# Kernel tuning notes

Measured on AMD Instinct MI355X. Metric: run time of the kernel, lower is better.

Reference implementation:

```python
import jax, jax.numpy as jnp
import numpy as np

EPS = 1e-6
N_HEADS = 16
D_HEAD = 64

def _rmsnorm(x, scale):
    rms = jnp.sqrt(jnp.mean(x * x, axis=-1, keepdims=True) + EPS)
    return x / rms * scale

def setup_inputs() -> dict:
    key = jax.random.key(0)
    ks = jax.random.split(key, 8)
    B, L, D = 512, 64, 1024
    return {
        "x": jax.random.normal(ks[0], (B, L, D), dtype=jnp.float32),
        "rel_indices": jax.random.randint(ks[1], (L, L), 0, 225, dtype=jnp.int64),
        "Wq": jax.random.normal(ks[2], (D, D), dtype=jnp.float32) * 0.02,
        "Wk": jax.random.normal(ks[3], (D, D), dtype=jnp.float32) * 0.02,
        "Wv": jax.random.normal(ks[4], (D, D), dtype=jnp.float32) * 0.02,
        "Wo": jax.random.normal(ks[5], (D, D), dtype=jnp.float32) * 0.02,
        "q_scale": jnp.ones((D_HEAD,), dtype=jnp.float32),
        "k_scale": jnp.ones((D_HEAD,), dtype=jnp.float32),
        "rel_k": jax.random.normal(ks[6], (225, D_HEAD), dtype=jnp.float32) * 0.02,
        "rel_v": jax.random.normal(ks[7], (225, D_HEAD), dtype=jnp.float32) * 0.02,
    }

def reference(x, rel_indices, Wq, Wk, Wv, Wo, q_scale, k_scale, rel_k, rel_v):
    B, L, D = x.shape
    H, dk = N_HEADS, D_HEAD
    scale = 1.0 / jnp.sqrt(jnp.float32(dk))
    # projections; Linear with weight W applied as x @ W (bias=False)
    q = (x @ Wq).reshape(B, L, H, dk)
    k = (x @ Wk).reshape(B, L, H, dk)
    v = (x @ Wv).reshape(B, L, H, dk).transpose(0, 2, 1, 3)  # bhld
    q = _rmsnorm(q, q_scale).transpose(0, 2, 1, 3)  # bhld
    k = _rmsnorm(k, k_scale).transpose(0, 2, 1, 3)  # bhld
    r_k = rel_k[rel_indices]  # [L, L, dk]
    r_v = rel_v[rel_indices]  # [L, L, dk]
    content = jnp.einsum('bhid,bhjd->bhij', q, k)
    rel = jnp.einsum('bhid,ijd->bhij', q, r_k)
    probs = jax.nn.softmax((content + rel) * scale, axis=-1)
    out = jnp.einsum('bhij,bhjd->bhid', probs, v) + jnp.einsum('bhij,ijd->bhid', probs, r_v)
    out = out.transpose(0, 2, 1, 3).reshape(B, L, D)
    return out @ Wo
```

## Files before the change

kernel.cpp:

```cpp
#include <hip/hip_runtime.h>
#include <stdint.h>

typedef unsigned short u16;
typedef __attribute__((ext_vector_type(8))) short s16x8;
typedef __attribute__((ext_vector_type(4))) float f32x4;

#define DEV static __device__ __forceinline__

#define MFMA16(a, b, c) __builtin_amdgcn_mfma_f32_16x16x32_bf16((a), (b), (c), 0, 0, 0)

DEV u16 f2b(float f) {
  unsigned u = __float_as_uint(f);
  unsigned r = (u + 0x7fffu + ((u >> 16) & 1u)) >> 16;
  return (u16)r;
}
DEV float b2f(u16 u) { return __uint_as_float(((unsigned)u) << 16); }

typedef const __attribute__((address_space(1))) unsigned int* as1p;
typedef __attribute__((address_space(3))) unsigned int* as3p;

DEV void gload16(const void* g, void* l) {
  __builtin_amdgcn_global_load_lds((as1p)(uintptr_t)g, (as3p)(unsigned)(uintptr_t)l, 16, 0, 0);
}

DEV void ldsPkAddBf16(void* ldsPtr, unsigned packed) {
  unsigned addr = (unsigned)(uintptr_t)ldsPtr;
  asm volatile("ds_pk_add_bf16 %0, %1" : : "v"(addr), "v"(packed) : "memory");
}

__global__ void conv_x_k(const float* __restrict__ x, u16* __restrict__ xb) {
  const int n8 = 32768 * 1024 / 8;
  int i = blockIdx.x * 256 + threadIdx.x;
  int stride = gridDim.x * 256;
  for (; i < n8; i += stride) {
    const float4* p = (const float4*)x + (size_t)i * 2;
    float4 a = p[0], c = p[1];
    union { s16x8 v; u16 u[8]; } o;
    o.u[0] = f2b(a.x); o.u[1] = f2b(a.y); o.u[2] = f2b(a.z); o.u[3] = f2b(a.w);
    o.u[4] = f2b(c.x); o.u[5] = f2b(c.y); o.u[6] = f2b(c.z); o.u[7] = f2b(c.w);
    *(s16x8*)(xb + (size_t)i * 8) = o.v;
  }
}

__global__ void transp_w_k(const float* __restrict__ Wq, const float* __restrict__ Wk,
                           const float* __restrict__ Wv, const float* __restrict__ Wo,
                           u16* __restrict__ wqkT, u16* __restrict__ wvT, u16* __restrict__ woT) {
  const int z = blockIdx.z;
  const float* src = z == 0 ? Wq : z == 1 ? Wk : z == 2 ? Wv : Wo;
  u16* dst = z == 0 ? wqkT : z == 1 ? (wqkT + 1024 * 1024) : z == 2 ? wvT : woT;
  __shared__ u16 t[64][72];
  const int kb = blockIdx.y * 64, nb = blockIdx.x * 64;
  const int tid = threadIdx.x;
  const int c = tid & 63, r0 = tid >> 6;
  #pragma unroll
  for (int s = 0; s < 16; ++s) {
    int r = r0 * 16 + s;
    t[r][c] = f2b(src[(size_t)(kb + r) * 1024 + nb + c]);
  }
  __syncthreads();
  #pragma unroll
  for (int s = 0; s < 16; ++s) {
    int n = r0 * 16 + s;
    dst[(size_t)(nb + n) * 1024 + kb + c] = t[c][n];
  }
}

__global__ void prep_rel_k(const float* __restrict__ rk, const float* __restrict__ rv,
                           u16* __restrict__ rkb, u16* __restrict__ rvT) {
  int i = blockIdx.x * 256 + threadIdx.x;
  if (i < 240 * 64) {
    int tt = i >> 6, d = i & 63;
    rkb[i] = (tt < 225) ? f2b(rk[tt * 64 + d]) : (u16)0;
  }
  if (i < 64 * 256) {
    int d = i >> 8, tt = i & 255;
    rvT[i] = (tt < 225) ? f2b(rv[tt * 64 + d]) : (u16)0;
  }
}

template <int EPI>
__global__ __launch_bounds__(256, 2)
void gemm_k(const u16* __restrict__ A, const u16* __restrict__ BT,
            u16* __restrict__ o16a, u16* __restrict__ o16b,
            float* __restrict__ oF,
            const float* __restrict__ qsc, const float* __restrict__ ksc) {
  __shared__ u16 smA[2][128 * 32];
  __shared__ u16 smB[2][128 * 32];
  const int tid = threadIdx.x;
  const int w = tid >> 6, l = tid & 63;
  const int lc = l & 15, l4 = l >> 4;
  const int nwg = gridDim.x * gridDim.y;
  const int orig = blockIdx.y * gridDim.x + blockIdx.x;
  const int wg = ((orig & 7) * (nwg >> 3)) + (orig >> 3);
  const int bx = wg % gridDim.x, by = wg / gridDim.x;
  const int m0 = by * 128, n0 = bx * 128;
  const int wm = (w >> 1) * 64, wn = (w & 1) * 64;

  f32x4 acc[4][4];
  #pragma unroll
  for (int i = 0; i < 4; ++i)
    #pragma unroll
    for (int j = 0; j < 4; ++j) acc[i][j] = (f32x4){0.f, 0.f, 0.f, 0.f};

  int srcRow[2], srcCol[2];
  #pragma unroll
  for (int s = 0; s < 2; ++s) {
    int p = w * 2048 + s * 1024 + l * 16;
    int row = p >> 6;
    int lb = p ^ (((row ^ (row >> 2)) & 3) << 4);
    srcRow[s] = row;
    srcCol[s] = (lb & 63) >> 1;
  }

  auto stage = [&](int buf, int kt) {
    #pragma unroll
    for (int s = 0; s < 2; ++s) {
      int base = w * 2048 + s * 1024;
      const u16* ga = A + (size_t)(m0 + srcRow[s]) * 1024 + kt * 32 + srcCol[s];
      gload16(ga, (char*)&smA[buf][0] + base);
      const u16* gb = BT + (size_t)(n0 + srcRow[s]) * 1024 + kt * 32 + srcCol[s];
      gload16(gb, (char*)&smB[buf][0] + base);
    }
  };
  auto fragA = [&](int buf, int mf) -> s16x8 {
    int row = wm + mf * 16 + lc;
    int p = (row << 6) + (l4 << 4);
    p ^= ((row ^ (row >> 2)) & 3) << 4;
    return *(const s16x8*)((const char*)&smA[buf][0] + p);
  };
  auto fragB = [&](int buf, int nf) -> s16x8 {
    int row = wn + nf * 16 + lc;
    int p = (row << 6) + (l4 << 4);
    p ^= ((row ^ (row >> 2)) & 3) << 4;
    return *(const s16x8*)((const char*)&smB[buf][0] + p);
  };

  stage(0, 0);
  __syncthreads();
  #pragma unroll 2
  for (int kt = 0; kt < 32; ++kt) {
    int cur = kt & 1;
    if (kt + 1 < 32) stage(cur ^ 1, kt + 1);
    s16x8 af[4], bf[4];
    #pragma unroll
    for (int i = 0; i < 4; ++i) { af[i] = fragA(cur, i); bf[i] = fragB(cur, i); }
    #pragma unroll
    for (int mf = 0; mf < 4; ++mf)
      #pragma unroll
      for (int nf = 0; nf < 4; ++nf)
        acc[mf][nf] = MFMA16(af[mf], bf[nf], acc[mf][nf]);
    __syncthreads();
  }

  if constexpr (EPI == 2) {
    #pragma unroll
    for (int mf = 0; mf < 4; ++mf)
      #pragma unroll
      for (int r = 0; r < 4; ++r) {
        int gm = m0 + wm + mf * 16 + l4 * 4 + r;
        #pragma unroll
        for (int nf = 0; nf < 4; ++nf) {
          int gn = n0 + wn + nf * 16 + lc;
          oF[(size_t)gm * 1024 + gn] = acc[mf][nf][r];
        }
      }
  } else if constexpr (EPI == 1) {
    #pragma unroll
    for (int mf = 0; mf < 4; ++mf)
      #pragma unroll
      for (int r = 0; r < 4; ++r) {
        int gm = m0 + wm + mf * 16 + l4 * 4 + r;
        #pragma unroll
        for (int nf = 0; nf < 4; ++nf) {
          int gn = n0 + wn + nf * 16 + lc;
          size_t addr = (((size_t)(gn >> 6) * 16 + (gm >> 6)) * 64 + (gm & 63)) * 64 + (gn & 63);
          o16a[addr] = f2b(acc[mf][nf][r]);
        }
      }
  } else {
    int nw0 = n0 + wn;
    bool isq = nw0 < 1024;
    const float* sc = isq ? qsc : ksc;
    u16* dst = isq ? o16a : o16b;
    int h = (nw0 & 1023) >> 6;
    float scv[4];
    #pragma unroll
    for (int nf = 0; nf < 4; ++nf) scv[nf] = sc[nf * 16 + lc];
    #pragma unroll
    for (int mf = 0; mf < 4; ++mf)
      #pragma unroll
      for (int r = 0; r < 4; ++r) {
        float ss = 0.f;
        #pragma unroll
        for (int nf = 0; nf < 4; ++nf) ss += acc[mf][nf][r] * acc[mf][nf][r];
        #pragma unroll
        for (int mask = 1; mask < 16; mask <<= 1) ss += __shfl_xor(ss, mask, 64);
        float rinv = rsqrtf(ss * 0.015625f + 1e-6f);
        int gm = m0 + wm + mf * 16 + l4 * 4 + r;
        size_t base = (((size_t)(gm >> 6) * 16 + h) * 64 + (gm & 63)) * 64;
        #pragma unroll
        for (int nf = 0; nf < 4; ++nf)
          dst[base + nf * 16 + lc] = f2b(acc[mf][nf][r] * rinv * scv[nf]);
      }
  }
}

DEV int rwByte(int row, int t) {
  return row * 512 + ((((t >> 3) ^ (row & 7)) << 4)) + ((t & 7) * 2);
}

__global__ __launch_bounds__(256, 2)
void attn_k(const u16* __restrict__ qn, const u16* __restrict__ kn,
            const u16* __restrict__ vT, const u16* __restrict__ rkb,
            const u16* __restrict__ rvT, const int* __restrict__ ridx,
            u16* __restrict__ ao) {
  __shared__ u16 Ksm[64 * 64];
  __shared__ u16 Vsm[64 * 64];
  __shared__ u16 RW[64 * 256];
  __shared__ u16 Pl[64 * 72];
  const int bid = blockIdx.x;
  const int b = bid >> 4, h = bid & 15;
  const int tid = threadIdx.x;
  const int w = tid >> 6, l = tid & 63;
  const int lc = l & 15, l4 = l >> 4;
  const int i0 = w * 16;
  const size_t hb = (size_t)(b * 16 + h) * 4096;
  const u16* qh = qn + hb;
  const u16* kh = kn + hb;
  const u16* vh = vT + hb;

  #pragma unroll
  for (int s = 0; s < 2; ++s) {
    int p = w * 2048 + s * 1024 + l * 16;
    int t = p >> 7;
    int sl = ((p >> 4) & 7) ^ (t & 7);
    int e = t * 64 + sl * 8;
    gload16(kh + e, (char*)Ksm + w * 2048 + s * 1024);
    gload16(vh + e, (char*)Vsm + w * 2048 + s * 1024);
  }

  int ts[4][4];
  #pragma unroll
  for (int q = 0; q < 4; ++q) {
    int row = i0 + l4 * 4 + q;
    #pragma unroll
    for (int nf = 0; nf < 4; ++nf) ts[nf][q] = ridx[row * 64 + nf * 16 + lc];
  }
  s16x8 aq0 = *(const s16x8*)(qh + (i0 + lc) * 64 + l4 * 8);
  s16x8 aq1 = *(const s16x8*)(qh + (i0 + lc) * 64 + 32 + l4 * 8);

  f32x4 accC[4];
  #pragma unroll
  for (int nf = 0; nf < 4; ++nf) accC[nf] = (f32x4){0.f, 0.f, 0.f, 0.f};

  {
    s16x8 rb0[15], rb1[15];
    #pragma unroll
    for (int u = 0; u < 15; ++u) {
      rb0[u] = *(const s16x8*)(rkb + (u * 16 + lc) * 64 + l4 * 8);
      rb1[u] = *(const s16x8*)(rkb + (u * 16 + lc) * 64 + 32 + l4 * 8);
    }
    __syncthreads();

    #pragma unroll
    for (int nf = 0; nf < 4; ++nf) {
      int row = nf * 16 + lc;
      s16x8 k0 = *(const s16x8*)((const char*)Ksm + row * 128 + (((0 + l4) ^ (row & 7)) << 4));
      s16x8 k1 = *(const s16x8*)((const char*)Ksm + row * 128 + (((4 + l4) ^ (row & 7)) << 4));
      accC[nf] = MFMA16(aq0, k0, accC[nf]);
      accC[nf] = MFMA16(aq1, k1, accC[nf]);
    }

    #pragma unroll
    for (int u = 0; u < 15; ++u) {
      f32x4 rr = (f32x4){0.f, 0.f, 0.f, 0.f};
      rr = MFMA16(aq0, rb0[u], rr);
      rr = MFMA16(aq1, rb1[u], rr);
      int t = u * 16 + lc;
      #pragma unroll
      for (int q = 0; q < 4; ++q) {
        int row = i0 + l4 * 4 + q;
        RW[rwByte(row, t) >> 1] = f2b(rr[q]);
      }
    }
  }
  __syncthreads();

  float ev[4][4];
  float linv[4];
  #pragma unroll
  for (int q = 0; q < 4; ++q) {
    int row = i0 + l4 * 4 + q;
    float mx = -1e30f;
    #pragma unroll
    for (int nf = 0; nf < 4; ++nf) {
      float r = b2f(RW[rwByte(row, ts[nf][q]) >> 1]);
      float s = (accC[nf][q] + r) * 0.125f;
      ev[nf][q] = s;
      mx = fmaxf(mx, s);
    }
    #pragma unroll
    for (int mask = 1; mask < 16; mask <<= 1) mx = fmaxf(mx, __shfl_xor(mx, mask, 64));
    float sum = 0.f;
    #pragma unroll
    for (int nf = 0; nf < 4; ++nf) { float e = __expf(ev[nf][q] - mx); ev[nf][q] = e; sum += e; }
    #pragma unroll
    for (int mask = 1; mask < 16; mask <<= 1) sum += __shfl_xor(sum, mask, 64);
    linv[q] = 1.f / sum;
    #pragma unroll
    for (int nf = 0; nf < 4; ++nf) Pl[row * 72 + nf * 16 + lc] = f2b(ev[nf][q]);
  }
  __syncthreads();

  s16x8 rvf[8][4];
  #pragma unroll
  for (int ks = 0; ks < 8; ++ks)
    #pragma unroll
    for (int nf = 0; nf < 4; ++nf)
      rvf[ks][nf] = *(const s16x8*)(rvT + (nf * 16 + lc) * 256 + ks * 32 + l4 * 8);
  {
    s16x8 z;
    #pragma unroll
    for (int j = 0; j < 8; ++j) z[j] = 0;
    #pragma unroll
    for (int zz = 0; zz < 8; ++zz) ((s16x8*)RW)[zz * 256 + tid] = z;
  }
  f32x4 accO[4];
  #pragma unroll
  for (int nf = 0; nf < 4; ++nf) accO[nf] = (f32x4){0.f, 0.f, 0.f, 0.f};
  s16x8 pa0 = *(const s16x8*)(&Pl[(i0 + lc) * 72 + l4 * 8]);
  s16x8 pa1 = *(const s16x8*)(&Pl[(i0 + lc) * 72 + 32 + l4 * 8]);
  #pragma unroll
  for (int nf = 0; nf < 4; ++nf) {
    int row = nf * 16 + lc;
    s16x8 v0 = *(const s16x8*)((const char*)Vsm + row * 128 + (((0 + l4) ^ (row & 7)) << 4));
    s16x8 v1 = *(const s16x8*)((const char*)Vsm + row * 128 + (((4 + l4) ^ (row & 7)) << 4));
    accO[nf] = MFMA16(pa0, v0, accO[nf]);
    accO[nf] = MFMA16(pa1, v1, accO[nf]);
  }
  __syncthreads();

  #pragma unroll
  for (int q = 0; q < 4; ++q)
    #pragma unroll
    for (int nf = 0; nf < 4; ++nf) {
      int row = i0 + l4 * 4 + q;
      int t = ts[nf][q];
      int byte = row * 512 + ((((t >> 3) ^ (row & 7)) << 4)) + ((t & 6) * 2);
      unsigned pk = ((unsigned)f2b(ev[nf][q])) << ((t & 1) * 16);
      ldsPkAddBf16((char*)RW + byte, pk);
    }
  asm volatile("s_waitcnt lgkmcnt(0)" ::: "memory");
  __syncthreads();

  #pragma unroll
  for (int ks = 0; ks < 8; ++ks) {
    int row = i0 + lc;
    s16x8 wa = *(const s16x8*)((const char*)RW + row * 512 + ((((ks * 4 + l4) ^ (row & 7))) << 4));
    #pragma unroll
    for (int nf = 0; nf < 4; ++nf)
      accO[nf] = MFMA16(wa, rvf[ks][nf], accO[nf]);
  }

  #pragma unroll
  for (int q = 0; q < 4; ++q) {
    int row = i0 + l4 * 4 + q;
    #pragma unroll
    for (int nf = 0; nf < 4; ++nf) {
      int d = nf * 16 + lc;
      ao[((size_t)(b * 64 + row)) * 1024 + h * 64 + d] = f2b(accO[nf][q] * linv[q]);
    }
  }
}

extern "C" void kernel_launch(void* const* d_in, const int* in_sizes, int n_in,
                              void* d_out, int out_size, void* d_ws, size_t ws_size,
                              hipStream_t stream) {
  (void)in_sizes; (void)n_in; (void)out_size; (void)ws_size;
  const float* x  = (const float*)d_in[0];
  const int* ridx = (const int*)d_in[1];
  const float* Wq = (const float*)d_in[2];
  const float* Wk = (const float*)d_in[3];
  const float* Wv = (const float*)d_in[4];
  const float* Wo = (const float*)d_in[5];
  const float* qs = (const float*)d_in[6];
  const float* ks = (const float*)d_in[7];
  const float* rk = (const float*)d_in[8];
  const float* rv = (const float*)d_in[9];
  float* out = (float*)d_out;

  char* ws = (char*)d_ws;
  const size_t SZ = 32768ull * 1024 * 2;
  u16* xb   = (u16*)(ws);
  u16* qn   = (u16*)(ws + SZ);
  u16* kn   = (u16*)(ws + 2 * SZ);
  u16* vT   = (u16*)(ws + 3 * SZ);
  u16* wqkT = (u16*)(ws + 4 * SZ);
  u16* wvT  = (u16*)(ws + 4 * SZ + 4194304);
  u16* woT  = (u16*)(ws + 4 * SZ + 6291456);
  u16* rkb  = (u16*)(ws + 4 * SZ + 8388608);
  u16* rvTb = (u16*)(ws + 4 * SZ + 8388608 + 30720);

  conv_x_k<<<2048, 256, 0, stream>>>(x, xb);
  transp_w_k<<<dim3(16, 16, 4), 256, 0, stream>>>(Wq, Wk, Wv, Wo, wqkT, wvT, woT);
  prep_rel_k<<<64, 256, 0, stream>>>(rk, rv, rkb, rvTb);
  gemm_k<0><<<dim3(16, 256), 256, 0, stream>>>(xb, wqkT, qn, kn, nullptr, qs, ks);
  gemm_k<1><<<dim3(256, 8), 256, 0, stream>>>(wvT, xb, vT, nullptr, nullptr, nullptr, nullptr);
  attn_k<<<8192, 256, 0, stream>>>(qn, kn, vT, rkb, rvTb, ridx, xb);
  gemm_k<2><<<dim3(8, 256), 256, 0, stream>>>(xb, woT, nullptr, nullptr, out, nullptr, nullptr);
}
```

Before: 955.6 us.

## Split attention into single-wave blocks per 16-row group, loading K/V directly

Restructures the attention kernel from one 256-thread block per (batch, head) into four 64-thread single-wave blocks, each handling 16 query rows. K and V fragments are now read straight from global memory instead of being staged through LDS, block-wide barriers become plain LDS waitcnts, and the grid is remapped so neighbouring blocks spread across the index space. The goal is to remove __syncthreads overhead, cut LDS use and raise occupancy. In exchange, each wave reloads the full K, V and rel tables from global memory, which multiplies L2 traffic by four.

```diff
diff --git a/kernel.cpp b/kernel.cpp
--- a/kernel.cpp
+++ b/kernel.cpp
@@ -26,6 +26,11 @@
 DEV void ldsPkAddBf16(void* ldsPtr, unsigned packed) {
   unsigned addr = (unsigned)(uintptr_t)ldsPtr;
   asm volatile("ds_pk_add_bf16 %0, %1" : : "v"(addr), "v"(packed) : "memory");
+}
+
+DEV void waitLds() {
+  asm volatile("s_waitcnt lgkmcnt(0)" ::: "memory");
+  __builtin_amdgcn_sched_barrier(0);
 }
 
 __global__ void conv_x_k(const float* __restrict__ x, u16* __restrict__ xb) {
@@ -209,93 +214,71 @@
   return row * 512 + ((((t >> 3) ^ (row & 7)) << 4)) + ((t & 7) * 2);
 }
 
-__global__ __launch_bounds__(256, 2)
+__global__ __launch_bounds__(64, 3)
 void attn_k(const u16* __restrict__ qn, const u16* __restrict__ kn,
             const u16* __restrict__ vT, const u16* __restrict__ rkb,
             const u16* __restrict__ rvT, const int* __restrict__ ridx,
             u16* __restrict__ ao) {
-  __shared__ u16 Ksm[64 * 64];
-  __shared__ u16 Vsm[64 * 64];
-  __shared__ u16 RW[64 * 256];
-  __shared__ u16 Pl[64 * 72];
-  const int bid = blockIdx.x;
-  const int b = bid >> 4, h = bid & 15;
-  const int tid = threadIdx.x;
-  const int w = tid >> 6, l = tid & 63;
+  __shared__ u16 RW[16 * 256];
+  __shared__ u16 Pl[16 * 72];
+  const int bid0 = blockIdx.x;
+  const int bid = (bid0 & 7) * 4096 + (bid0 >> 3);
+  const int rg = bid & 3, h = (bid >> 2) & 15, b = bid >> 6;
+  const int i0 = rg * 16;
+  const int l = threadIdx.x;
   const int lc = l & 15, l4 = l >> 4;
-  const int i0 = w * 16;
   const size_t hb = (size_t)(b * 16 + h) * 4096;
   const u16* qh = qn + hb;
   const u16* kh = kn + hb;
   const u16* vh = vT + hb;
 
-  #pragma unroll
-  for (int s = 0; s < 2; ++s) {
-    int p = w * 2048 + s * 1024 + l * 16;
-    int t = p >> 7;
-    int sl = ((p >> 4) & 7) ^ (t & 7);
-    int e = t * 64 + sl * 8;
-    gload16(kh + e, (char*)Ksm + w * 2048 + s * 1024);
-    gload16(vh + e, (char*)Vsm + w * 2048 + s * 1024);
-  }
-
-  int ts[4][4];
-  #pragma unroll
-  for (int q = 0; q < 4; ++q) {
-    int row = i0 + l4 * 4 + q;
-    #pragma unroll
-    for (int nf = 0; nf < 4; ++nf) ts[nf][q] = ridx[row * 64 + nf * 16 + lc];
-  }
   s16x8 aq0 = *(const s16x8*)(qh + (i0 + lc) * 64 + l4 * 8);
   s16x8 aq1 = *(const s16x8*)(qh + (i0 + lc) * 64 + 32 + l4 * 8);
 
   f32x4 accC[4];
   #pragma unroll
   for (int nf = 0; nf < 4; ++nf) accC[nf] = (f32x4){0.f, 0.f, 0.f, 0.f};
-
-  {
-    s16x8 rb0[15], rb1[15];
-    #pragma unroll
-    for (int u = 0; u < 15; ++u) {
-      rb0[u] = *(const s16x8*)(rkb + (u * 16 + lc) * 64 + l4 * 8);
-      rb1[u] = *(const s16x8*)(rkb + (u * 16 + lc) * 64 + 32 + l4 * 8);
-    }
-    __syncthreads();
-
-    #pragma unroll
-    for (int nf = 0; nf < 4; ++nf) {
-      int row = nf * 16 + lc;
-      s16x8 k0 = *(const s16x8*)((const char*)Ksm + row * 128 + (((0 + l4) ^ (row & 7)) << 4));
-      s16x8 k1 = *(const s16x8*)((const char*)Ksm + row * 128 + (((4 + l4) ^ (row & 7)) << 4));
-      accC[nf] = MFMA16(aq0, k0, accC[nf]);
-      accC[nf] = MFMA16(aq1, k1, accC[nf]);
-    }
-
-    #pragma unroll
-    for (int u = 0; u < 15; ++u) {
-      f32x4 rr = (f32x4){0.f, 0.f, 0.f, 0.f};
-      rr = MFMA16(aq0, rb0[u], rr);
-      rr = MFMA16(aq1, rb1[u], rr);
-      int t = u * 16 + lc;
-      #pragma unroll
-      for (int q = 0; q < 4; ++q) {
-        int row = i0 + l4 * 4 + q;
-        RW[rwByte(row, t) >> 1] = f2b(rr[q]);
-      }
-    }
-  }
-  __syncthreads();
-
+  #pragma unroll
+  for (int nf = 0; nf < 4; ++nf) {
+    s16x8 k0 = *(const s16x8*)(kh + (nf * 16 + lc) * 64 + l4 * 8);
+    s16x8 k1 = *(const s16x8*)(kh + (nf * 16 + lc) * 64 + 32 + l4 * 8);
+    accC[nf] = MFMA16(aq0, k0, accC[nf]);
+    accC[nf] = MFMA16(aq1, k1, accC[nf]);
+  }
+
+  #pragma unroll
+  for (int u = 0; u < 15; ++u) {
+    s16x8 rb0 = *(const s16x8*)(rkb + (u * 16 + lc) * 64 + l4 * 8);
+    s16x8 rb1 = *(const s16x8*)(rkb + (u * 16 + lc) * 64 + 32 + l4 * 8);
+    f32x4 rr = (f32x4){0.f, 0.f, 0.f, 0.f};
+    rr = MFMA16(aq0, rb0, rr);
+    rr = MFMA16(aq1, rb1, rr);
+    int t = u * 16 + lc;
+    #pragma unroll
+    for (int q = 0; q < 4; ++q) {
+      int r = l4 * 4 + q;
+      RW[rwByte(r, t) >> 1] = f2b(rr[q]);
+    }
+  }
+  waitLds();
+
+  int ts[4][4];
+  #pragma unroll
+  for (int q = 0; q < 4; ++q) {
+    int grow = i0 + l4 * 4 + q;
+    #pragma unroll
+    for (int nf = 0; nf < 4; ++nf) ts[nf][q] = ridx[grow * 64 + nf * 16 + lc];
+  }
   float ev[4][4];
   float linv[4];
   #pragma unroll
   for (int q = 0; q < 4; ++q) {
-    int row = i0 + l4 * 4 + q;
+    int r = l4 * 4 + q;
     float mx = -1e30f;
     #pragma unroll
     for (int nf = 0; nf < 4; ++nf) {
-      float r = b2f(RW[rwByte(row, ts[nf][q]) >> 1]);
-      float s = (accC[nf][q] + r) * 0.125f;
+      float rv = b2f(RW[rwByte(r, ts[nf][q]) >> 1]);
+      float s = (accC[nf][q] + rv) * 0.125f;
       ev[nf][q] = s;
       mx = fmaxf(mx, s);
     }
@@ -308,67 +291,61 @@
     for (int mask = 1; mask < 16; mask <<= 1) sum += __shfl_xor(sum, mask, 64);
     linv[q] = 1.f / sum;
     #pragma unroll
-    for (int nf = 0; nf < 4; ++nf) Pl[row * 72 + nf * 16 + lc] = f2b(ev[nf][q]);
-  }
-  __syncthreads();
-
-  s16x8 rvf[8][4];
-  #pragma unroll
-  for (int ks = 0; ks < 8; ++ks)
-    #pragma unroll
-    for (int nf = 0; nf < 4; ++nf)
-      rvf[ks][nf] = *(const s16x8*)(rvT + (nf * 16 + lc) * 256 + ks * 32 + l4 * 8);
+    for (int nf = 0; nf < 4; ++nf) Pl[r * 72 + nf * 16 + lc] = f2b(ev[nf][q]);
+  }
+  waitLds();
+
   {
     s16x8 z;
     #pragma unroll
     for (int j = 0; j < 8; ++j) z[j] = 0;
     #pragma unroll
-    for (int zz = 0; zz < 8; ++zz) ((s16x8*)RW)[zz * 256 + tid] = z;
-  }
+    for (int zz = 0; zz < 8; ++zz) ((s16x8*)RW)[zz * 64 + l] = z;
+  }
+  s16x8 pa0 = *(const s16x8*)(&Pl[lc * 72 + l4 * 8]);
+  s16x8 pa1 = *(const s16x8*)(&Pl[lc * 72 + 32 + l4 * 8]);
   f32x4 accO[4];
   #pragma unroll
   for (int nf = 0; nf < 4; ++nf) accO[nf] = (f32x4){0.f, 0.f, 0.f, 0.f};
-  s16x8 pa0 = *(const s16x8*)(&Pl[(i0 + lc) * 72 + l4 * 8]);
-  s16x8 pa1 = *(const s16x8*)(&Pl[(i0 + lc) * 72 + 32 + l4 * 8]);
   #pragma unroll
   for (int nf = 0; nf < 4; ++nf) {
-    int row = nf * 16 + lc;
-    s16x8 v0 = *(const s16x8*)((const char*)Vsm + row * 128 + (((0 + l4) ^ (row & 7)) << 4));
-    s16x8 v1 = *(const s16x8*)((const char*)Vsm + row * 128 + (((4 + l4) ^ (row & 7)) << 4));
+    s16x8 v0 = *(const s16x8*)(vh + (nf * 16 + lc) * 64 + l4 * 8);
+    s16x8 v1 = *(const s16x8*)(vh + (nf * 16 + lc) * 64 + 32 + l4 * 8);
     accO[nf] = MFMA16(pa0, v0, accO[nf]);
     accO[nf] = MFMA16(pa1, v1, accO[nf]);
   }
-  __syncthreads();
+  waitLds();
 
   #pragma unroll
   for (int q = 0; q < 4; ++q)
     #pragma unroll
     for (int nf = 0; nf < 4; ++nf) {
-      int row = i0 + l4 * 4 + q;
+      int r = l4 * 4 + q;
       int t = ts[nf][q];
-      int byte = row * 512 + ((((t >> 3) ^ (row & 7)) << 4)) + ((t & 6) * 2);
+      int byte = r * 512 + ((((t >> 3) ^ (r & 7)) << 4)) + ((t & 6) * 2);
       unsigned pk = ((unsigned)f2b(ev[nf][q])) << ((t & 1) * 16);
       ldsPkAddBf16((char*)RW + byte, pk);
     }
-  asm volatile("s_waitcnt lgkmcnt(0)" ::: "memory");
-  __syncthreads();
+  waitLds();
 
   #pragma unroll
   for (int ks = 0; ks < 8; ++ks) {
-    int row = i0 + lc;
-    s16x8 wa = *(const s16x8*)((const char*)RW + row * 512 + ((((ks * 4 + l4) ^ (row & 7))) << 4));
-    #pragma unroll
-    for (int nf = 0; nf < 4; ++nf)
-      accO[nf] = MFMA16(wa, rvf[ks][nf], accO[nf]);
+    int r = lc;
+    s16x8 wa = *(const s16x8*)((const char*)RW + r * 512 + ((((ks * 4 + l4) ^ (r & 7))) << 4));
+    #pragma unroll
+    for (int nf = 0; nf < 4; ++nf) {
+      s16x8 rb = *(const s16x8*)(rvT + (nf * 16 + lc) * 256 + ks * 32 + l4 * 8);
+      accO[nf] = MFMA16(wa, rb, accO[nf]);
+    }
   }
 
   #pragma unroll
   for (int q = 0; q < 4; ++q) {
-    int row = i0 + l4 * 4 + q;
+    int grow = i0 + l4 * 4 + q;
     #pragma unroll
     for (int nf = 0; nf < 4; ++nf) {
       int d = nf * 16 + lc;
-      ao[((size_t)(b * 64 + row)) * 1024 + h * 64 + d] = f2b(accO[nf][q] * linv[q]);
+      ao[((size_t)(b * 64 + grow)) * 1024 + h * 64 + d] = f2b(accO[nf][q] * linv[q]);
     }
   }
 }
@@ -406,6 +383,6 @@
   prep_rel_k<<<64, 256, 0, stream>>>(rk, rv, rkb, rvTb);
   gemm_k<0><<<dim3(16, 256), 256, 0, stream>>>(xb, wqkT, qn, kn, nullptr, qs, ks);
   gemm_k<1><<<dim3(256, 8), 256, 0, stream>>>(wvT, xb, vT, nullptr, nullptr, nullptr, nullptr);
-  attn_k<<<8192, 256, 0, stream>>>(qn, kn, vT, rkb, rvTb, ridx, xb);
+  attn_k<<<32768, 64, 0, stream>>>(qn, kn, vT, rkb, rvTb, ridx, xb);
   gemm_k<2><<<dim3(8, 256), 256, 0, stream>>>(xb, woT, nullptr, nullptr, out, nullptr, nullptr);
 }
```

Measured after the change: 894.3 us. 1.07x faster.
